# Kernel tuning notes

Hardware: AMD Instinct MI355X
Metric: run time of the kernel (lower is better)

Reference implementation:

```python
import jax, jax.numpy as jnp
import numpy as np

B, D_IN, L = 16, 16, 4096
H, N2, NL = 256, 32, 4


def setup_inputs() -> dict:
    key = jax.random.key(0)
    ks = jax.random.split(key, 16)
    log_dt = jnp.log(0.001) + jax.random.uniform(ks[3], (NL, H)) * (jnp.log(0.1) - jnp.log(0.001))
    return {
        "x": jax.random.normal(ks[0], (B, D_IN, L), jnp.float32),
        "enc_w": jax.random.normal(ks[1], (D_IN, H), jnp.float32) / np.sqrt(D_IN),
        "enc_b": jax.random.normal(ks[2], (H,), jnp.float32) * 0.01,
        "log_dt": log_dt.astype(jnp.float32),
        "A_re": jax.random.normal(ks[4], (NL, H, N2), jnp.float32) * 0.5,
        "A_im": jax.random.normal(ks[5], (NL, H, N2), jnp.float32) * np.pi,
        "C_re": jax.random.normal(ks[6], (NL, H, N2), jnp.float32),
        "C_im": jax.random.normal(ks[7], (NL, H, N2), jnp.float32),
        "D": jax.random.normal(ks[8], (NL, H), jnp.float32),
        "W_out": jax.random.normal(ks[9], (NL, H, H), jnp.float32) / np.sqrt(H),
        "b_out": jax.random.normal(ks[10], (NL, H), jnp.float32) * 0.01,
        "ln_w": jnp.ones((NL, H), jnp.float32),
        "ln_b": jnp.zeros((NL, H), jnp.float32),
        "dec_w": jax.random.normal(ks[11], (H, D_IN), jnp.float32) / np.sqrt(H),
        "dec_b": jax.random.normal(ks[12], (D_IN,), jnp.float32) * 0.01,
    }


def _s4_layer(z, log_dt, A_re, A_im, C_re, C_im, D, W_out, b_out):
    # z: (B, H, L). Diagonal SSM (S4D) with ZOH discretization + FFT causal conv.
    Ltot = z.shape[-1]
    dt = jnp.exp(log_dt)                              # (H,)
    A = -jnp.exp(A_re) + 1j * A_im                    # (H, N2) complex, Re<0
    C = C_re + 1j * C_im                              # (H, N2)
    dtA = A * dt[:, None]                             # (H, N2)
    Cc = C * (jnp.exp(dtA) - 1.0) / A                 # discretized C*B coefficients
    # Vandermonde: K[h,l] = 2*Re(sum_n Cc[h,n] * exp(dtA[h,n]*l))
    t = jnp.arange(Ltot)
    vand = jnp.exp(dtA[:, :, None] * t)               # (H, N2, L) complex
    K = 2.0 * jnp.einsum('hn,hnl->hl', Cc, vand).real # (H, L)
    nfft = 2 * Ltot
    y = jnp.fft.irfft(jnp.fft.rfft(z, n=nfft) * jnp.fft.rfft(K, n=nfft)[None], n=nfft)[..., :Ltot]
    y = y + z * D[None, :, None]                      # skip term
    y = jax.nn.gelu(y)                                # final_act='gelu'
    y = jnp.einsum('bhl,hd->bdl', y, W_out) + b_out[None, :, None]  # pointwise output linear
    return y


def _layernorm(x_bhl, w, b):
    # LayerNorm over channel dim H of (B, H, L)
    mu = jnp.mean(x_bhl, axis=1, keepdims=True)
    var = jnp.var(x_bhl, axis=1, keepdims=True)
    xn = (x_bhl - mu) * jax.lax.rsqrt(var + 1e-5)
    return xn * w[None, :, None] + b[None, :, None]


def reference(x, enc_w, enc_b, log_dt, A_re, A_im, C_re, C_im, D, W_out, b_out, ln_w, ln_b, dec_w, dec_b):
    # encoder: (B, d_in, L) -> (B, H, L)
    h = jnp.einsum('bil,ih->bhl', x, enc_w) + enc_b[None, :, None]
    for i in range(NL):
        z = _s4_layer(h, log_dt[i], A_re[i], A_im[i], C_re[i], C_im[i], D[i], W_out[i], b_out[i])
        h = z + h
        h = _layernorm(h, ln_w[i], ln_b[i])  # post-norm (prenorm=False)
    out = jnp.einsum('bhl,hd->bdl', h, dec_w) + dec_b[None, :, None]
    return out
```

## Files before the change

### kernel.cpp

```cpp
#include <hip/hip_runtime.h>
#include <hip/hip_bf16.h>
#include <math.h>

#define Bb 16
#define DIN 16
#define LL 4096
#define HH 256
#define NN2 32
#define NLAY 4
#define HN (HH*NN2)
#define BN 32

typedef __attribute__((ext_vector_type(8))) short short8;
typedef __attribute__((ext_vector_type(4))) short short4v;
typedef __attribute__((ext_vector_type(4))) float f32x4;
typedef unsigned short u16;

__device__ inline u16 f2bf(float f) {
  unsigned int x = __float_as_uint(f);
  unsigned int r = x + 0x7FFFu + ((x >> 16) & 1u);
  return (u16)(r >> 16);
}
__device__ inline float bf2f(u16 u) {
  return __uint_as_float(((unsigned int)u) << 16);
}
__device__ inline unsigned int packsplit(float v) {
  u16 hi = f2bf(v);
  u16 lo = f2bf(v - bf2f(hi));
  return (((unsigned int)hi) << 16) | lo;
}
__device__ inline unsigned int cvtpk(float a, float b) {
  unsigned int r;
  asm("v_cvt_pk_bf16_f32 %0, %1, %2" : "=v"(r) : "v"(a), "v"(b));
  return r;
}
__device__ inline short8 ld8(const u16* p) {
  short4v a = *(const short4v*)p;
  short4v b = *(const short4v*)(p + 16);
  return __builtin_shufflevector(a, b, 0, 1, 2, 3, 4, 5, 6, 7);
}
__device__ inline size_t fidx(int h, int m, int row, int col) {
  int wv = row >> 4, row16 = row & 15;
  int kh = col >> 5, c5 = col & 31;
  int lane = ((c5 & 15) >> 2) * 16 + row16;
  int j = (((c5 >> 4) & 1) << 2) | (c5 & 3);
  return ((((((size_t)h * 6 + m) * 4 + wv) * 2 + kh) * 64 + lane) << 3) + j;
}

__global__ __launch_bounds__(256) void enc_kernel(const float* __restrict__ x,
    const float* __restrict__ ew, const float* __restrict__ eb,
    float* __restrict__ hbuf) {
  int blk = blockIdx.x;
  int tile = blk & 15;
  int h = (blk >> 4) & (HH - 1);
  int b = blk >> 12;
  int l = tile * 256 + threadIdx.x;
  const float* xb = x + (size_t)b * DIN * LL + l;
  float acc = eb[h];
  #pragma unroll
  for (int i = 0; i < DIN; ++i)
    acc = fmaf(xb[(size_t)i * LL], ew[i * HH + h], acc);
  hbuf[((size_t)(b * HH + h)) * LL + l] = acc;
}

__global__ __launch_bounds__(256) void basis_kernel(
    const float* __restrict__ log_dt, const float* __restrict__ Are,
    const float* __restrict__ Aim, const float* __restrict__ Cre,
    const float* __restrict__ Cim, float* __restrict__ w64,
    u16* __restrict__ Bf) {
  __shared__ float K_l[64];
  int h = blockIdx.x;
  int t = threadIdx.x;
  if (t < 32) {
    int n = t;
    int idx = h * 32 + n;
    float dt = expf(log_dt[h]);
    float ar = -expf(Are[idx]);
    float ai = Aim[idx];
    float er = expf(ar * dt);
    float wr = er * cosf(ai * dt);
    float wi = er * sinf(ai * dt);
    float nr = wr - 1.f, ni = wi;
    float inv = 1.f / (ar * ar + ai * ai);
    float qr = (nr * ar + ni * ai) * inv;
    float qi = (ni * ar - nr * ai) * inv;
    float crv = Cre[idx], civ = Cim[idx];
    float cr = 2.f * (crv * qr - civ * qi);
    float ci = 2.f * (crv * qi + civ * qr);
    float pr = wr, pi = wi;
    #pragma unroll
    for (int q = 0; q < 6; ++q) {
      float t0 = pr * pr - pi * pi;
      pi = 2.f * pr * pi;
      pr = t0;
    }
    w64[idx] = pr;
    w64[HN + idx] = pi;
    float vr = 1.f, vi = 0.f;
    for (int m = 0; m <= 64; ++m) {
      float e = cr * vr - ci * vi;
      float f = -(cr * vi + ci * vr);
      float s = e;
      s += __shfl_xor(s, 1); s += __shfl_xor(s, 2); s += __shfl_xor(s, 4);
      s += __shfl_xor(s, 8); s += __shfl_xor(s, 16);
      if (m <= 63) {
        if (n == 0) K_l[m] = s;
        int i = 63 - m;
        u16 hr = f2bf(vr);
        Bf[fidx(h, 2, 2 * n, i)] = hr;
        Bf[fidx(h, 3, 2 * n, i)] = f2bf(vr - bf2f(hr));
        u16 hi2 = f2bf(vi);
        Bf[fidx(h, 2, 2 * n + 1, i)] = hi2;
        Bf[fidx(h, 3, 2 * n + 1, i)] = f2bf(vi - bf2f(hi2));
      }
      if (m >= 1) {
        int row = m - 1;
        u16 he = f2bf(e);
        Bf[fidx(h, 4, row, 2 * n)] = he;
        Bf[fidx(h, 5, row, 2 * n)] = f2bf(e - bf2f(he));
        u16 hf = f2bf(f);
        Bf[fidx(h, 4, row, 2 * n + 1)] = hf;
        Bf[fidx(h, 5, row, 2 * n + 1)] = f2bf(f - bf2f(hf));
      }
      float nvr = vr * wr - vi * wi;
      float nvi = vr * wi + vi * wr;
      vr = nvr; vi = nvi;
    }
  }
  __syncthreads();
  #pragma unroll
  for (int p = 0; p < 16; ++p) {
    int id = p * 256 + t;
    int j = id >> 6, i = id & 63;
    float kv = (j >= i) ? K_l[j - i] : 0.f;
    u16 hi = f2bf(kv);
    Bf[fidx(h, 0, j, i)] = hi;
    Bf[fidx(h, 1, j, i)] = f2bf(kv - bf2f(hi));
  }
}

__global__ __launch_bounds__(256) void wpack_kernel(const float* __restrict__ W,
                                                    unsigned int* __restrict__ Wp) {
  int idx = blockIdx.x * 256 + threadIdx.x;
  int j = idx & 7;
  int lane = (idx >> 3) & 63;
  int di = (idx >> 9) & 3;
  int ks = (idx >> 11) & 7;
  int wv = idx >> 14;
  int row16 = lane & 15, kgrp = lane >> 4;
  int d = wv * 64 + di * 16 + row16;
  int hcol = ks * 32 + kgrp * 4 + (j & 3) + ((j >> 2) << 4);
  Wp[idx] = packsplit(W[hcol * HH + d]);
}

__global__ __launch_bounds__(256, 4) void s4_mfma_kernel(
    const float* __restrict__ zg, const float* __restrict__ w64,
    const float* __restrict__ Dvec, const u16* __restrict__ Bf,
    unsigned int* __restrict__ gout) {
  __shared__ u16 zh[64 * 68], zl[64 * 68];
  __shared__ float stT[64 * 68];
  u16* sh = (u16*)stT;
  u16* sl = sh + 64 * 68;
  unsigned int* packbuf = (unsigned int*)stT;
  int bh = blockIdx.x, h = bh & (HH - 1), t = threadIdx.x;
  int wv = t >> 6, lane = t & 63, row16 = lane & 15, kgrp = lane >> 4;
  const u16* BfH = Bf + (size_t)h * (6 * 4 * 2 * 64 * 8);
  #define LDF(m, kh) (*(const short8*)(BfH + (((m) * 4 + wv) * 2 + (kh)) * 512 + lane * 8))
  short8 fTh0 = LDF(0, 0), fTh1 = LDF(0, 1);
  short8 fTl0 = LDF(1, 0), fTl1 = LDF(1, 1);
  short8 fMh0 = LDF(2, 0), fMh1 = LDF(2, 1);
  short8 fMl0 = LDF(3, 0), fMl1 = LDF(3, 1);
  const float* zrow = zg + (size_t)bh * LL;
  int c0 = t >> 2, i0 = (t & 3) * 16;
  {
    const float4* zsrc = (const float4*)(zrow + c0 * 64 + i0);
    #pragma unroll
    for (int q = 0; q < 4; ++q) {
      float4 v = zsrc[q];
      unsigned int hp0 = cvtpk(v.x, v.y);
      unsigned int hp1 = cvtpk(v.z, v.w);
      float r0 = v.x - __uint_as_float(hp0 << 16);
      float r1 = v.y - __uint_as_float(hp0 & 0xFFFF0000u);
      float r2 = v.z - __uint_as_float(hp1 << 16);
      float r3 = v.w - __uint_as_float(hp1 & 0xFFFF0000u);
      unsigned int lp0 = cvtpk(r0, r1);
      unsigned int lp1 = cvtpk(r2, r3);
      int base = c0 * 68 + i0 + q * 4;
      *(unsigned int*)&zh[base] = hp0;
      *(unsigned int*)&zh[base + 2] = hp1;
      *(unsigned int*)&zl[base] = lp0;
      *(unsigned int*)&zl[base + 2] = lp1;
    }
  }
  __syncthreads();
  f32x4 y[4];
  #pragma unroll
  for (int ct = 0; ct < 4; ++ct) {
    f32x4 aS = (f32x4){0.f, 0.f, 0.f, 0.f};
    f32x4 aY = (f32x4){0.f, 0.f, 0.f, 0.f};
    int cc = ct * 16 + row16;
    #pragma unroll
    for (int kh = 0; kh < 2; ++kh) {
      int kb = kh * 32 + kgrp * 4;
      short8 Bh = ld8(&zh[cc * 68 + kb]);
      short8 Bl = ld8(&zl[cc * 68 + kb]);
      short8 Ah = kh ? fMh1 : fMh0;
      short8 Al = kh ? fMl1 : fMl0;
      aS = __builtin_amdgcn_mfma_f32_16x16x32_bf16(Ah, Bh, aS, 0, 0, 0);
      aS = __builtin_amdgcn_mfma_f32_16x16x32_bf16(Ah, Bl, aS, 0, 0, 0);
      aS = __builtin_amdgcn_mfma_f32_16x16x32_bf16(Al, Bh, aS, 0, 0, 0);
      short8 Ch = kh ? fTh1 : fTh0;
      short8 Cl = kh ? fTl1 : fTl0;
      aY = __builtin_amdgcn_mfma_f32_16x16x32_bf16(Ch, Bh, aY, 0, 0, 0);
      aY = __builtin_amdgcn_mfma_f32_16x16x32_bf16(Ch, Bl, aY, 0, 0, 0);
      aY = __builtin_amdgcn_mfma_f32_16x16x32_bf16(Cl, Bh, aY, 0, 0, 0);
    }
    y[ct] = aY;
    #pragma unroll
    for (int r = 0; r < 4; ++r)
      stT[(wv * 16 + kgrp * 4 + r) * 68 + cc] = aS[r];
  }
  __syncthreads();
  short8 fEh0 = LDF(4, 0), fEh1 = LDF(4, 1);
  short8 fEl0 = LDF(5, 0), fEl1 = LDF(5, 1);
  #undef LDF
  float ir[8], ii[8];
  {
    float xr[8], xi[8], pr[8], pi[8];
    #pragma unroll
    for (int k = 0; k < 8; ++k) {
      int d0 = wv * 16 + 2 * k;
      xr[k] = stT[d0 * 68 + lane];
      xi[k] = stT[(d0 + 1) * 68 + lane];
      pr[k] = w64[h * 32 + wv * 8 + k];
      pi[k] = w64[HN + h * 32 + wv * 8 + k];
    }
    #pragma unroll
    for (int d = 1; d < 64; d <<= 1) {
      #pragma unroll
      for (int k = 0; k < 8; ++k) {
        float qr = __shfl_up(xr[k], d);
        float qi = __shfl_up(xi[k], d);
        if (lane >= d) {
          xr[k] = fmaf(pr[k], qr, fmaf(-pi[k], qi, xr[k]));
          xi[k] = fmaf(pr[k], qi, fmaf(pi[k], qr, xi[k]));
        }
        float t0 = pr[k] * pr[k] - pi[k] * pi[k];
        pi[k] = 2.f * pr[k] * pi[k];
        pr[k] = t0;
      }
    }
    #pragma unroll
    for (int k = 0; k < 8; ++k) {
      ir[k] = __shfl_up(xr[k], 1);
      ii[k] = __shfl_up(xi[k], 1);
      if (lane == 0) { ir[k] = 0.f; ii[k] = 0.f; }
    }
  }
  __syncthreads();
  #pragma unroll
  for (int k = 0; k < 8; ++k) {
    int d0 = wv * 16 + 2 * k;
    unsigned int hp = cvtpk(ir[k], ii[k]);
    float rr = ir[k] - __uint_as_float(hp << 16);
    float ri = ii[k] - __uint_as_float(hp & 0xFFFF0000u);
    unsigned int lp = cvtpk(rr, ri);
    *(unsigned int*)&sh[lane * 68 + d0] = hp;
    *(unsigned int*)&sl[lane * 68 + d0] = lp;
  }
  __syncthreads();
  #pragma unroll
  for (int ct = 0; ct < 4; ++ct) {
    f32x4 a = y[ct];
    int cc = ct * 16 + row16;
    #pragma unroll
    for (int kh = 0; kh < 2; ++kh) {
      int kb = kh * 32 + kgrp * 4;
      short8 Sh8 = ld8(&sh[cc * 68 + kb]);
      short8 Sl8 = ld8(&sl[cc * 68 + kb]);
      short8 Ah = kh ? fEh1 : fEh0;
      short8 Al = kh ? fEl1 : fEl0;
      a = __builtin_amdgcn_mfma_f32_16x16x32_bf16(Ah, Sh8, a, 0, 0, 0);
      a = __builtin_amdgcn_mfma_f32_16x16x32_bf16(Ah, Sl8, a, 0, 0, 0);
      a = __builtin_amdgcn_mfma_f32_16x16x32_bf16(Al, Sh8, a, 0, 0, 0);
    }
    y[ct] = a;
  }
  __syncthreads();
  {
    float Dh = Dvec[h];
    int j0 = wv * 16 + kgrp * 4;
    #pragma unroll
    for (int ct = 0; ct < 4; ++ct) {
      int cc = ct * 16 + row16;
      unsigned int za = *(const unsigned int*)&zh[cc * 68 + j0];
      unsigned int zb = *(const unsigned int*)&zh[cc * 68 + j0 + 2];
      unsigned int la = *(const unsigned int*)&zl[cc * 68 + j0];
      unsigned int lb = *(const unsigned int*)&zl[cc * 68 + j0 + 2];
      float zf[4];
      zf[0] = __uint_as_float(za << 16) + __uint_as_float(la << 16);
      zf[1] = __uint_as_float(za & 0xFFFF0000u) + __uint_as_float(la & 0xFFFF0000u);
      zf[2] = __uint_as_float(zb << 16) + __uint_as_float(lb << 16);
      zf[3] = __uint_as_float(zb & 0xFFFF0000u) + __uint_as_float(lb & 0xFFFF0000u);
      float v[4];
      #pragma unroll
      for (int r = 0; r < 4; ++r) {
        float vv = fmaf(zf[r], Dh, y[ct][r]);
        float u = 1.5957691216057308f * fmaf(0.044715f * vv, vv * vv, vv);
        v[r] = vv / (1.f + __expf(-u));
      }
      unsigned int h01 = cvtpk(v[0], v[1]);
      unsigned int h23 = cvtpk(v[2], v[3]);
      float r0 = v[0] - __uint_as_float(h01 << 16);
      float r1 = v[1] - __uint_as_float(h01 & 0xFFFF0000u);
      float r2 = v[2] - __uint_as_float(h23 << 16);
      float r3 = v[3] - __uint_as_float(h23 & 0xFFFF0000u);
      unsigned int l01 = cvtpk(r0, r1);
      unsigned int l23 = cvtpk(r2, r3);
      uint4 w;
      w.x = (h01 << 16) | (l01 & 0xFFFFu);
      w.y = (h01 & 0xFFFF0000u) | (l01 >> 16);
      w.z = (h23 << 16) | (l23 & 0xFFFFu);
      w.w = (h23 & 0xFFFF0000u) | (l23 >> 16);
      *(uint4*)&packbuf[cc * 68 + j0] = w;
    }
  }
  __syncthreads();
  {
    unsigned int* grow = gout + (size_t)bh * LL;
    #pragma unroll
    for (int q = 0; q < 4; ++q) {
      uint4 v = *(const uint4*)&packbuf[c0 * 68 + i0 + q * 4];
      *(uint4*)&grow[c0 * 64 + i0 + q * 4] = v;
    }
  }
}

__global__ __launch_bounds__(256, 4) void mm_mfma_ln_kernel(
    const unsigned int* __restrict__ gp, float* __restrict__ h_buf,
    const unsigned int* __restrict__ Wp, const float* __restrict__ bo,
    const float* __restrict__ lw, const float* __restrict__ lb) {
  __shared__ unsigned int gt[BN * HH];
  __shared__ float red_s[4][BN];
  __shared__ float red_q[4][BN];
  int blk = blockIdx.x;
  int b = blk >> 7;
  int l0 = (blk & 127) * BN;
  int t = threadIdx.x;
  const unsigned int* gbase = gp + (size_t)b * HH * LL + l0;
  #pragma unroll
  for (int p = 0; p < 4; ++p) {
    int hh = p * 64 + (t >> 2);
    int lq = (t & 3) * 8;
    const uint4* src = (const uint4*)(gbase + (size_t)hh * LL + lq);
    uint4 v0 = src[0];
    uint4 v1 = src[1];
    unsigned int vals[8] = {v0.x, v0.y, v0.z, v0.w, v1.x, v1.y, v1.z, v1.w};
    #pragma unroll
    for (int j = 0; j < 8; ++j) {
      int l = lq + j;
      int xm = (l & 7) ^ ((l >> 3) & 3);
      int g4 = (hh >> 2) ^ xm;
      gt[l * HH + g4 * 4 + (hh & 3)] = vals[j];
    }
  }
  __syncthreads();
  int wv = t >> 6, lane = t & 63;
  int row16 = lane & 15, kgrp = lane >> 4;
  f32x4 acc[4][2];
  #pragma unroll
  for (int di = 0; di < 4; ++di)
    #pragma unroll
    for (int li = 0; li < 2; ++li)
      acc[di][li] = (f32x4){0.f, 0.f, 0.f, 0.f};
  #pragma unroll 2
  for (int ks = 0; ks < 8; ++ks) {
    int h0 = ks * 32;
    short8 Bhi[2], Blo[2];
    #pragma unroll
    for (int li = 0; li < 2; ++li) {
      int l = li * 16 + row16;
      int xm = (l & 7) ^ ((l >> 3) & 3);
      int g4a = ((h0 >> 2) + kgrp) ^ xm;
      int g4b = ((h0 >> 2) + kgrp + 4) ^ xm;
      uint4 pa = *(const uint4*)&gt[l * HH + g4a * 4];
      uint4 pb = *(const uint4*)&gt[l * HH + g4b * 4];
      union { int i[4]; short8 s; } uh, ul;
      uh.i[0] = (int)((pa.x >> 16) | (pa.y & 0xFFFF0000u));
      uh.i[1] = (int)((pa.z >> 16) | (pa.w & 0xFFFF0000u));
      uh.i[2] = (int)((pb.x >> 16) | (pb.y & 0xFFFF0000u));
      uh.i[3] = (int)((pb.z >> 16) | (pb.w & 0xFFFF0000u));
      ul.i[0] = (int)((pa.x & 0xFFFFu) | (pa.y << 16));
      ul.i[1] = (int)((pa.z & 0xFFFFu) | (pa.w << 16));
      ul.i[2] = (int)((pb.x & 0xFFFFu) | (pb.y << 16));
      ul.i[3] = (int)((pb.z & 0xFFFFu) | (pb.w << 16));
      Bhi[li] = uh.s; Blo[li] = ul.s;
    }
    #pragma unroll
    for (int di = 0; di < 4; ++di) {
      const uint4* wf = (const uint4*)Wp + ((((wv * 8 + ks) * 4 + di) * 64 + lane) * 2);
      uint4 pa = wf[0];
      uint4 pb = wf[1];
      union { int i[4]; short8 s; } uh, ul;
      uh.i[0] = (int)((pa.x >> 16) | (pa.y & 0xFFFF0000u));
      uh.i[1] = (int)((pa.z >> 16) | (pa.w & 0xFFFF0000u));
      uh.i[2] = (int)((pb.x >> 16) | (pb.y & 0xFFFF0000u));
      uh.i[3] = (int)((pb.z >> 16) | (pb.w & 0xFFFF0000u));
      ul.i[0] = (int)((pa.x & 0xFFFFu) | (pa.y << 16));
      ul.i[1] = (int)((pa.z & 0xFFFFu) | (pa.w << 16));
      ul.i[2] = (int)((pb.x & 0xFFFFu) | (pb.y << 16));
      ul.i[3] = (int)((pb.z & 0xFFFFu) | (pb.w << 16));
      short8 Ahi = uh.s, Alo = ul.s;
      #pragma unroll
      for (int li = 0; li < 2; ++li) {
        acc[di][li] = __builtin_amdgcn_mfma_f32_16x16x32_bf16(Ahi, Bhi[li], acc[di][li], 0, 0, 0);
        acc[di][li] = __builtin_amdgcn_mfma_f32_16x16x32_bf16(Ahi, Blo[li], acc[di][li], 0, 0, 0);
        acc[di][li] = __builtin_amdgcn_mfma_f32_16x16x32_bf16(Alo, Bhi[li], acc[di][li], 0, 0, 0);
      }
    }
  }
  const float* hb = h_buf + (size_t)b * HH * LL + l0;
  #pragma unroll
  for (int di = 0; di < 4; ++di) {
    #pragma unroll
    for (int r = 0; r < 4; ++r) {
      int d = wv * 64 + di * 16 + kgrp * 4 + r;
      float bov = bo[d];
      #pragma unroll
      for (int li = 0; li < 2; ++li) {
        int l = li * 16 + row16;
        acc[di][li][r] += bov + hb[(size_t)d * LL + l];
      }
    }
  }
  #pragma unroll
  for (int li = 0; li < 2; ++li) {
    float s = 0.f, q = 0.f;
    #pragma unroll
    for (int di = 0; di < 4; ++di)
      #pragma unroll
      for (int r = 0; r < 4; ++r) {
        float v = acc[di][li][r];
        s += v;
        q = fmaf(v, v, q);
      }
    s += __shfl_xor(s, 16); s += __shfl_xor(s, 32);
    q += __shfl_xor(q, 16); q += __shfl_xor(q, 32);
    if (lane < 16) {
      red_s[wv][li * 16 + lane] = s;
      red_q[wv][li * 16 + lane] = q;
    }
  }
  __syncthreads();
  float mu[2], rstd[2];
  #pragma unroll
  for (int li = 0; li < 2; ++li) {
    int cl = li * 16 + row16;
    float s = red_s[0][cl] + red_s[1][cl] + red_s[2][cl] + red_s[3][cl];
    float q = red_q[0][cl] + red_q[1][cl] + red_q[2][cl] + red_q[3][cl];
    float m = s * (1.f / 256.f);
    float var = q * (1.f / 256.f) - m * m;
    mu[li] = m;
    rstd[li] = rsqrtf(var + 1e-5f);
  }
  float* hw = h_buf + (size_t)b * HH * LL + l0;
  #pragma unroll
  for (int di = 0; di < 4; ++di) {
    #pragma unroll
    for (int r = 0; r < 4; ++r) {
      int d = wv * 64 + di * 16 + kgrp * 4 + r;
      float lwv = lw[d], lbv = lb[d];
      #pragma unroll
      for (int li = 0; li < 2; ++li) {
        int l = li * 16 + row16;
        hw[(size_t)d * LL + l] = (acc[di][li][r] - mu[li]) * rstd[li] * lwv + lbv;
      }
    }
  }
}

__global__ __launch_bounds__(256) void dec_kernel(
    const float* __restrict__ hbuf, const float* __restrict__ dw,
    const float* __restrict__ db, float* __restrict__ outp) {
  __shared__ float dwl[HH * DIN];
  int blk = blockIdx.x;
  int b = blk >> 4;
  int l0 = (blk & 15) * 256;
  int t = threadIdx.x;
  #pragma unroll
  for (int p = 0; p < 16; ++p) dwl[p * 256 + t] = dw[p * 256 + t];
  __syncthreads();
  float acc[DIN];
  #pragma unroll
  for (int d = 0; d < DIN; ++d) acc[d] = db[d];
  const float* hb = hbuf + (size_t)b * HH * LL + l0;
  for (int hh = 0; hh < HH; ++hh) {
    float v = hb[(size_t)hh * LL + t];
    #pragma unroll
    for (int d = 0; d < DIN; ++d)
      acc[d] = fmaf(v, dwl[hh * DIN + d], acc[d]);
  }
  float* ob = outp + (size_t)b * DIN * LL + l0;
  #pragma unroll
  for (int d = 0; d < DIN; ++d) ob[(size_t)d * LL + t] = acc[d];
}

extern "C" void kernel_launch(void* const* d_in, const int* in_sizes, int n_in,
                              void* d_out, int out_size, void* d_ws, size_t ws_size,
                              hipStream_t stream) {
  const float* x      = (const float*)d_in[0];
  const float* enc_w  = (const float*)d_in[1];
  const float* enc_b  = (const float*)d_in[2];
  const float* log_dt = (const float*)d_in[3];
  const float* A_re   = (const float*)d_in[4];
  const float* A_im   = (const float*)d_in[5];
  const float* C_re   = (const float*)d_in[6];
  const float* C_im   = (const float*)d_in[7];
  const float* Dv     = (const float*)d_in[8];
  const float* W_out  = (const float*)d_in[9];
  const float* b_out  = (const float*)d_in[10];
  const float* ln_w   = (const float*)d_in[11];
  const float* ln_b   = (const float*)d_in[12];
  const float* dec_w  = (const float*)d_in[13];
  const float* dec_b  = (const float*)d_in[14];
  float* out = (float*)d_out;

  float* h_buf = (float*)d_ws;
  unsigned int* g_pack = (unsigned int*)(h_buf + (size_t)Bb * HH * LL);
  float* w64 = (float*)(g_pack + (size_t)Bb * HH * LL);
  unsigned int* Wp = (unsigned int*)(w64 + 2 * HN);
  u16* Bf = (u16*)(Wp + HH * HH);

  enc_kernel<<<Bb * HH * (LL / 256), 256, 0, stream>>>(x, enc_w, enc_b, h_buf);
  for (int i = 0; i < NLAY; ++i) {
    basis_kernel<<<HH, 256, 0, stream>>>(log_dt + i * HH, A_re + i * HN,
                                         A_im + i * HN, C_re + i * HN,
                                         C_im + i * HN, w64, Bf);
    wpack_kernel<<<HH * HH / 256, 256, 0, stream>>>(W_out + (size_t)i * HH * HH, Wp);
    s4_mfma_kernel<<<Bb * HH, 256, 0, stream>>>(h_buf, w64, Dv + i * HH, Bf, g_pack);
    mm_mfma_ln_kernel<<<Bb * (LL / BN), 256, 0, stream>>>(
        g_pack, h_buf, Wp, b_out + i * HH, ln_w + i * HH, ln_b + i * HH);
  }
  dec_kernel<<<Bb * (LL / 256), 256, 0, stream>>>(h_buf, dec_w, dec_b, out);
}
```

Baseline: 647.2 us.

## Fold D skip into Toeplitz diagonal, presplit W, stage residual/LN through LDS

```diff
diff --git a/kernel.cpp b/kernel.cpp
--- a/kernel.cpp
+++ b/kernel.cpp
@@ -66,8 +66,8 @@
 __global__ __launch_bounds__(256) void basis_kernel(
     const float* __restrict__ log_dt, const float* __restrict__ Are,
     const float* __restrict__ Aim, const float* __restrict__ Cre,
-    const float* __restrict__ Cim, float* __restrict__ w64,
-    u16* __restrict__ Bf) {
+    const float* __restrict__ Cim, const float* __restrict__ Dvec,
+    float* __restrict__ w64, u16* __restrict__ Bf) {
   __shared__ float K_l[64];
   int h = blockIdx.x;
   int t = threadIdx.x;
@@ -128,11 +128,13 @@
     }
   }
   __syncthreads();
+  float Dh = Dvec[h];
   #pragma unroll
   for (int p = 0; p < 16; ++p) {
     int id = p * 256 + t;
     int j = id >> 6, i = id & 63;
     float kv = (j >= i) ? K_l[j - i] : 0.f;
+    if (j == i) kv += Dh;
     u16 hi = f2bf(kv);
     Bf[fidx(h, 0, j, i)] = hi;
     Bf[fidx(h, 1, j, i)] = f2bf(kv - bf2f(hi));
@@ -140,7 +142,8 @@
 }
 
 __global__ __launch_bounds__(256) void wpack_kernel(const float* __restrict__ W,
-                                                    unsigned int* __restrict__ Wp) {
+                                                    u16* __restrict__ Whf,
+                                                    u16* __restrict__ Wlf) {
   int idx = blockIdx.x * 256 + threadIdx.x;
   int j = idx & 7;
   int lane = (idx >> 3) & 63;
@@ -150,13 +153,15 @@
   int row16 = lane & 15, kgrp = lane >> 4;
   int d = wv * 64 + di * 16 + row16;
   int hcol = ks * 32 + kgrp * 4 + (j & 3) + ((j >> 2) << 4);
-  Wp[idx] = packsplit(W[hcol * HH + d]);
+  float w = W[hcol * HH + d];
+  u16 hi = f2bf(w);
+  Whf[idx] = hi;
+  Wlf[idx] = f2bf(w - bf2f(hi));
 }
 
 __global__ __launch_bounds__(256, 4) void s4_mfma_kernel(
     const float* __restrict__ zg, const float* __restrict__ w64,
-    const float* __restrict__ Dvec, const u16* __restrict__ Bf,
-    unsigned int* __restrict__ gout) {
+    const u16* __restrict__ Bf, unsigned int* __restrict__ gout) {
   __shared__ u16 zh[64 * 68], zl[64 * 68];
   __shared__ float stT[64 * 68];
   u16* sh = (u16*)stT;
@@ -288,24 +293,14 @@
   }
   __syncthreads();
   {
-    float Dh = Dvec[h];
     int j0 = wv * 16 + kgrp * 4;
     #pragma unroll
     for (int ct = 0; ct < 4; ++ct) {
       int cc = ct * 16 + row16;
-      unsigned int za = *(const unsigned int*)&zh[cc * 68 + j0];
-      unsigned int zb = *(const unsigned int*)&zh[cc * 68 + j0 + 2];
-      unsigned int la = *(const unsigned int*)&zl[cc * 68 + j0];
-      unsigned int lb = *(const unsigned int*)&zl[cc * 68 + j0 + 2];
-      float zf[4];
-      zf[0] = __uint_as_float(za << 16) + __uint_as_float(la << 16);
-      zf[1] = __uint_as_float(za & 0xFFFF0000u) + __uint_as_float(la & 0xFFFF0000u);
-      zf[2] = __uint_as_float(zb << 16) + __uint_as_float(lb << 16);
-      zf[3] = __uint_as_float(zb & 0xFFFF0000u) + __uint_as_float(lb & 0xFFFF0000u);
       float v[4];
       #pragma unroll
       for (int r = 0; r < 4; ++r) {
-        float vv = fmaf(zf[r], Dh, y[ct][r]);
+        float vv = y[ct][r];
         float u = 1.5957691216057308f * fmaf(0.044715f * vv, vv * vv, vv);
         v[r] = vv / (1.f + __expf(-u));
       }
@@ -338,16 +333,27 @@
 
 __global__ __launch_bounds__(256, 4) void mm_mfma_ln_kernel(
     const unsigned int* __restrict__ gp, float* __restrict__ h_buf,
-    const unsigned int* __restrict__ Wp, const float* __restrict__ bo,
-    const float* __restrict__ lw, const float* __restrict__ lb) {
-  __shared__ unsigned int gt[BN * HH];
+    const u16* __restrict__ Whf, const u16* __restrict__ Wlf,
+    const float* __restrict__ bo, const float* __restrict__ lw,
+    const float* __restrict__ lb) {
+  __shared__ float smem[HH * 33];
   __shared__ float red_s[4][BN];
   __shared__ float red_q[4][BN];
+  unsigned int* gt = (unsigned int*)smem;
+  float* rt = smem;
   int blk = blockIdx.x;
   int b = blk >> 7;
   int l0 = (blk & 127) * BN;
   int t = threadIdx.x;
   const unsigned int* gbase = gp + (size_t)b * HH * LL + l0;
+  const float* hbp = h_buf + (size_t)b * HH * LL + l0;
+  float4 res[8];
+  #pragma unroll
+  for (int p = 0; p < 8; ++p) {
+    int row = p * 32 + (t >> 3);
+    int c4 = (t & 7) * 4;
+    res[p] = *(const float4*)(hbp + (size_t)row * LL + c4);
+  }
   #pragma unroll
   for (int p = 0; p < 4; ++p) {
     int hh = p * 64 + (t >> 2);
@@ -398,19 +404,9 @@
     }
     #pragma unroll
     for (int di = 0; di < 4; ++di) {
-      const uint4* wf = (const uint4*)Wp + ((((wv * 8 + ks) * 4 + di) * 64 + lane) * 2);
-      uint4 pa = wf[0];
-      uint4 pb = wf[1];
-      union { int i[4]; short8 s; } uh, ul;
-      uh.i[0] = (int)((pa.x >> 16) | (pa.y & 0xFFFF0000u));
-      uh.i[1] = (int)((pa.z >> 16) | (pa.w & 0xFFFF0000u));
-      uh.i[2] = (int)((pb.x >> 16) | (pb.y & 0xFFFF0000u));
-      uh.i[3] = (int)((pb.z >> 16) | (pb.w & 0xFFFF0000u));
-      ul.i[0] = (int)((pa.x & 0xFFFFu) | (pa.y << 16));
-      ul.i[1] = (int)((pa.z & 0xFFFFu) | (pa.w << 16));
-      ul.i[2] = (int)((pb.x & 0xFFFFu) | (pb.y << 16));
-      ul.i[3] = (int)((pb.z & 0xFFFFu) | (pb.w << 16));
-      short8 Ahi = uh.s, Alo = ul.s;
+      size_t fo = ((size_t)((wv * 8 + ks) * 4 + di) * 64 + lane) * 8;
+      short8 Ahi = *(const short8*)(Whf + fo);
+      short8 Alo = *(const short8*)(Wlf + fo);
       #pragma unroll
       for (int li = 0; li < 2; ++li) {
         acc[di][li] = __builtin_amdgcn_mfma_f32_16x16x32_bf16(Ahi, Bhi[li], acc[di][li], 0, 0, 0);
@@ -419,7 +415,16 @@
       }
     }
   }
-  const float* hb = h_buf + (size_t)b * HH * LL + l0;
+  __syncthreads();
+  #pragma unroll
+  for (int p = 0; p < 8; ++p) {
+    int row = p * 32 + (t >> 3);
+    int c4 = (t & 7) * 4;
+    float* dst = &rt[row * 33 + c4];
+    dst[0] = res[p].x; dst[1] = res[p].y; dst[2] = res[p].z; dst[3] = res[p].w;
+  }
+  __syncthreads();
+  float vv[4][2][4];
   #pragma unroll
   for (int di = 0; di < 4; ++di) {
     #pragma unroll
@@ -429,7 +434,7 @@
       #pragma unroll
       for (int li = 0; li < 2; ++li) {
         int l = li * 16 + row16;
-        acc[di][li][r] += bov + hb[(size_t)d * LL + l];
+        vv[di][li][r] = acc[di][li][r] + bov + rt[d * 33 + l];
       }
     }
   }
@@ -440,7 +445,7 @@
     for (int di = 0; di < 4; ++di)
       #pragma unroll
       for (int r = 0; r < 4; ++r) {
-        float v = acc[di][li][r];
+        float v = vv[di][li][r];
         s += v;
         q = fmaf(v, v, q);
       }
@@ -463,7 +468,6 @@
     mu[li] = m;
     rstd[li] = rsqrtf(var + 1e-5f);
   }
-  float* hw = h_buf + (size_t)b * HH * LL + l0;
   #pragma unroll
   for (int di = 0; di < 4; ++di) {
     #pragma unroll
@@ -473,9 +477,20 @@
       #pragma unroll
       for (int li = 0; li < 2; ++li) {
         int l = li * 16 + row16;
-        hw[(size_t)d * LL + l] = (acc[di][li][r] - mu[li]) * rstd[li] * lwv + lbv;
-      }
-    }
+        rt[d * 33 + l] = (vv[di][li][r] - mu[li]) * rstd[li] * lwv + lbv;
+      }
+    }
+  }
+  __syncthreads();
+  float* hw = h_buf + (size_t)b * HH * LL + l0;
+  #pragma unroll
+  for (int p = 0; p < 8; ++p) {
+    int row = p * 32 + (t >> 3);
+    int c4 = (t & 7) * 4;
+    const float* src = &rt[row * 33 + c4];
+    float4 v;
+    v.x = src[0]; v.y = src[1]; v.z = src[2]; v.w = src[3];
+    *(float4*)(hw + (size_t)row * LL + c4) = v;
   }
 }
 
@@ -528,18 +543,19 @@
   float* h_buf = (float*)d_ws;
   unsigned int* g_pack = (unsigned int*)(h_buf + (size_t)Bb * HH * LL);
   float* w64 = (float*)(g_pack + (size_t)Bb * HH * LL);
-  unsigned int* Wp = (unsigned int*)(w64 + 2 * HN);
-  u16* Bf = (u16*)(Wp + HH * HH);
+  u16* Whf = (u16*)(w64 + 2 * HN);
+  u16* Wlf = Whf + HH * HH;
+  u16* Bf = Wlf + HH * HH;
 
   enc_kernel<<<Bb * HH * (LL / 256), 256, 0, stream>>>(x, enc_w, enc_b, h_buf);
   for (int i = 0; i < NLAY; ++i) {
     basis_kernel<<<HH, 256, 0, stream>>>(log_dt + i * HH, A_re + i * HN,
                                          A_im + i * HN, C_re + i * HN,
-                                         C_im + i * HN, w64, Bf);
-    wpack_kernel<<<HH * HH / 256, 256, 0, stream>>>(W_out + (size_t)i * HH * HH, Wp);
-    s4_mfma_kernel<<<Bb * HH, 256, 0, stream>>>(h_buf, w64, Dv + i * HH, Bf, g_pack);
+                                         C_im + i * HN, Dv + i * HH, w64, Bf);
+    wpack_kernel<<<HH * HH / 256, 256, 0, stream>>>(W_out + (size_t)i * HH * HH, Whf, Wlf);
+    s4_mfma_kernel<<<Bb * HH, 256, 0, stream>>>(h_buf, w64, Bf, g_pack);
     mm_mfma_ln_kernel<<<Bb * (LL / BN), 256, 0, stream>>>(
-        g_pack, h_buf, Wp, b_out + i * HH, ln_w + i * HH, ln_b + i * HH);
+        g_pack, h_buf, Whf, Wlf, b_out + i * HH, ln_w + i * HH, ln_b + i * HH);
   }
   dec_kernel<<<Bb * (LL / 256), 256, 0, stream>>>(h_buf, dec_w, dec_b, out);
 }
```

New measurement: 681.1 us. 1.05x slower.
